# Performance work log

Hardware: AMD Instinct MI355X
Metric: run time of the kernel (lower is better)

Reference implementation:

```python
import jax, jax.numpy as jnp
import numpy as np

N_SEQ = 250000
L = 40
C_IN = 20
K = 4
D = 32
N_BAGS = 100
SEQ_PER_BAG = N_SEQ // N_BAGS


def _param(key, shape):
    # matches torch init: normal(0, sqrt(1/prod(shape)))
    return jax.random.normal(key, shape, dtype=jnp.float32) * np.sqrt(1.0 / np.prod(shape))


def setup_inputs() -> dict:
    key = jax.random.key(0)
    ks = jax.random.split(key, 16)
    inp = {
        "x": jax.random.normal(ks[0], (N_SEQ, L, C_IN), dtype=jnp.float32),
        # equal-size bags: 100 bags of 2500 sequences (sum == N_SEQ)
        "n_per_bag": jnp.full((N_BAGS,), SEQ_PER_BAG, dtype=jnp.int32),
        # CNN: two conv1d layers, kernel shape (K, in, out) for 'NWC'/'WIO'
        "conv1_w": _param(ks[1], (K, C_IN, D)), "conv1_b": jnp.zeros((D,), jnp.float32),
        "conv2_w": _param(ks[2], (K, D, D)),    "conv2_b": jnp.zeros((D,), jnp.float32),
        # attention MLP: 32->32->32->1
        "att_w1": _param(ks[3], (D, D)), "att_b1": jnp.zeros((D,), jnp.float32),
        "att_w2": _param(ks[4], (D, D)), "att_b2": jnp.zeros((D,), jnp.float32),
        "att_w3": _param(ks[5], (D, 1)), "att_b3": jnp.zeros((1,), jnp.float32),
        # output net A: 32->32->21, output net B: 32->32->40
        "outA_w1": _param(ks[6], (D, D)),  "outA_b1": jnp.zeros((D,), jnp.float32),
        "outA_w2": _param(ks[7], (D, 21)), "outA_b2": jnp.zeros((21,), jnp.float32),
        "outB_w1": _param(ks[8], (D, D)),  "outB_b1": jnp.zeros((D,), jnp.float32),
        "outB_w2": _param(ks[9], (D, 40)), "outB_b2": jnp.zeros((40,), jnp.float32),
    }
    return inp


def _conv1d_nwc(x, w, b):
    # x: (N, L, Cin), w: (K, Cin, Cout) -> (N, L-K+1, Cout), VALID padding
    return jax.lax.conv_general_dilated(
        x, w, window_strides=(1,), padding="VALID",
        dimension_numbers=("NWC", "WIO", "NWC")) + b


def _forward(x, n_per_bag, conv1_w, conv1_b, conv2_w, conv2_b,
             att_w1, att_b1, att_w2, att_b2, att_w3, att_b3,
             outA_w1, outA_b1, outA_w2, outA_b2,
             outB_w1, outB_b1, outB_w2, outB_b2):
    selu = jax.nn.selu
    # --- sequence embedding CNN (dropout = identity in eval) ---
    h = selu(_conv1d_nwc(x, conv1_w, conv1_b))          # (N, L-3, D)
    h = selu(_conv1d_nwc(h, conv2_w, conv2_b))          # (N, L-6, D)
    seq_embed = h.max(axis=1)                           # (N, D)
    # --- attention scores ---
    a = selu(seq_embed @ att_w1 + att_b1)
    a = selu(a @ att_w2 + att_b2)
    scores = (a @ att_w3 + att_b3)[:, 0]                # (N,)
    # --- per-bag segment softmax + weighted-sum pooling ---
    seg = jnp.repeat(jnp.arange(N_BAGS, dtype=jnp.int32), np.asarray(n_per_bag),
                     total_repeat_length=seq_embed.shape[0])
    seg_max = jax.ops.segment_max(scores, seg, num_segments=N_BAGS)
    e = jnp.exp(scores - seg_max[seg])
    denom = jax.ops.segment_sum(e, seg, num_segments=N_BAGS)
    w = e / denom[seg]                                  # (N,)
    pooled = jax.ops.segment_sum(seq_embed * w[:, None], seg,
                                 num_segments=N_BAGS)   # (N_BAGS, D)
    # --- output networks (n_layers=2: one hidden SELU layer + final, then sigmoid) ---
    pa = jax.nn.sigmoid(selu(pooled @ outA_w1 + outA_b1) @ outA_w2 + outA_b2)
    pb = jax.nn.sigmoid(selu(pooled @ outB_w1 + outB_b1) @ outB_w2 + outB_b2)
    return pa, pb


def reference(x, n_per_bag, conv1_w, conv1_b, conv2_w, conv2_b,
              att_w1, att_b1, att_w2, att_b2, att_w3, att_b3,
              outA_w1, outA_b1, outA_w2, outA_b2,
              outB_w1, outB_b1, outB_w2, outB_b2):
    return _forward(x, n_per_bag, conv1_w, conv1_b, conv2_w, conv2_b,
                    att_w1, att_b1, att_w2, att_b2, att_w3, att_b3,
                    outA_w1, outA_b1, outA_w2, outA_b2,
                    outB_w1, outB_b1, outB_w2, outB_b2)
```

## Files before the change

### kernel.cpp

```cpp
#include <hip/hip_runtime.h>

#define N_SEQ 250000
#define LSEQ  40
#define CIN   20
#define KW    4
#define DCH   32
#define L1    37
#define L2    34
#define N_BAGS 100
#define SPB   2500
#define NTHR  256
#define WPB   4
#define H1S   40

typedef _Float16 f16;
typedef _Float16 f16x8 __attribute__((ext_vector_type(8)));
typedef _Float16 f16x4 __attribute__((ext_vector_type(4)));
typedef float    f32x16 __attribute__((ext_vector_type(16)));

__device__ __forceinline__ float selu_f(float x) {
  float e = 1.6732632423543772f * (__expf(x) - 1.0f);
  return 1.0507009873554805f * ((x > 0.0f) ? x : e);
}

__device__ __forceinline__ float lane_bcast(float v, int srclane) {
  return __int_as_float(__builtin_amdgcn_readlane(__float_as_int(v), srclane));
}

__global__ __launch_bounds__(256) void prep_kernel(
    const float* __restrict__ w1, const float* __restrict__ w2,
    const float* __restrict__ aw1, const float* __restrict__ aw2,
    f16* __restrict__ w1T, f16* __restrict__ w2T,
    float* __restrict__ aw1T, float* __restrict__ aw2T)
{
  const int tid = threadIdx.x;
  for (int i = tid; i < 32 * 80; i += 256) {
    const int n = i / 80, k = i - n * 80;
    w1T[i] = (f16)w1[k * 32 + n];
  }
  for (int i = tid; i < 32 * 128; i += 256) {
    const int n = i >> 7, k = i & 127;
    w2T[i] = (f16)w2[k * 32 + n];
  }
  for (int i = tid; i < 1024; i += 256) {
    const int d = i >> 5, c = i & 31;
    aw1T[i] = aw1[c * 32 + d];
    aw2T[i] = aw2[c * 32 + d];
  }
}

__global__ __launch_bounds__(NTHR, 4) void seq_kernel(
    const float* __restrict__ x,
    const f16*  __restrict__ w1T, const float* __restrict__ b1,
    const f16*  __restrict__ w2T, const float* __restrict__ b2,
    const float* __restrict__ aw1T, const float* __restrict__ ab1,
    const float* __restrict__ aw2T, const float* __restrict__ ab2,
    const float* __restrict__ aw3, const float* __restrict__ ab3,
    f16* __restrict__ se_out, float* __restrict__ sc_out)
{
  __shared__ __align__(16) f16 xs[WPB][LSEQ * CIN];
  __shared__ __align__(16) f16 h1[WPB][L1 * H1S];

  const int tid  = threadIdx.x;
  const int lane = tid & 63;
  const int wave = tid >> 6;
  const int m    = lane & 31;
  const int half = lane >> 5;
  const int seq  = blockIdx.x * WPB + wave;

  f16* xw  = xs[wave];
  f16* h1w = h1[wave];

  {
    const float4* xg = (const float4*)(x + (size_t)seq * (LSEQ * CIN));
    for (int i = lane; i < 100; i += 64) {
      const float4 v0 = xg[2 * i];
      const float4 v1 = xg[2 * i + 1];
      f16x8 h;
      h[0] = (f16)v0.x; h[1] = (f16)v0.y; h[2] = (f16)v0.z; h[3] = (f16)v0.w;
      h[4] = (f16)v1.x; h[5] = (f16)v1.y; h[6] = (f16)v1.z; h[7] = (f16)v1.w;
      *(f16x8*)&xw[i * 8] = h;
    }
  }

  f16x8 bf1[5];
  {
    const f16x8* w1t8 = (const f16x8*)w1T;
    #pragma unroll
    for (int kc = 0; kc < 5; kc++) bf1[kc] = w1t8[m * 10 + kc * 2 + half];
  }
  const float b1v = b1[m];

  #pragma unroll
  for (int tile = 0; tile < 2; tile++) {
    const int l = tile ? min(32 + m, L1 - 1) : m;
    const f16* arow = &xw[l * CIN];
    f32x16 acc;
    #pragma unroll
    for (int i = 0; i < 16; i++) acc[i] = b1v;
    #pragma unroll
    for (int kc = 0; kc < 5; kc++) {
      const int e = kc * 16 + half * 8;
      const f16x4 p0 = *(const f16x4*)(arow + e);
      const f16x4 p1 = *(const f16x4*)(arow + e + 4);
      const f16x8 a = __builtin_shufflevector(p0, p1, 0, 1, 2, 3, 4, 5, 6, 7);
      acc = __builtin_amdgcn_mfma_f32_32x32x16_f16(a, bf1[kc], acc, 0, 0, 0);
    }
    if (tile == 0) {
      #pragma unroll
      for (int reg = 0; reg < 16; reg++) {
        const int rr = (reg & 3) + 8 * (reg >> 2) + 4 * half;
        h1w[rr * H1S + m] = (f16)selu_f(acc[reg]);
      }
    } else {
      if (half == 0) {
        #pragma unroll
        for (int reg = 0; reg < 4; reg++)
          h1w[(32 + reg) * H1S + m] = (f16)selu_f(acc[reg]);
      } else {
        h1w[36 * H1S + m] = (f16)selu_f(acc[0]);
      }
    }
  }

  f16x8 bf2[8];
  {
    const f16x8* w2t8 = (const f16x8*)w2T;
    #pragma unroll
    for (int kc = 0; kc < 8; kc++) bf2[kc] = w2t8[m * 16 + kc * 2 + half];
  }
  const float b2v = b2[m];

  float mx = -3.4e38f;
  #pragma unroll
  for (int tile = 0; tile < 2; tile++) {
    const int l = tile ? min(32 + m, L2 - 1) : m;
    const f16* abase = &h1w[l * H1S];
    f32x16 acc;
    #pragma unroll
    for (int i = 0; i < 16; i++) acc[i] = 0.0f;
    #pragma unroll
    for (int kc = 0; kc < 8; kc++) {
      const int e = (kc >> 1) * H1S + (kc & 1) * 16 + half * 8;
      const f16x8 a = *(const f16x8*)(abase + e);
      acc = __builtin_amdgcn_mfma_f32_32x32x16_f16(a, bf2[kc], acc, 0, 0, 0);
    }
    if (tile == 0) {
      #pragma unroll
      for (int reg = 0; reg < 16; reg++) mx = fmaxf(mx, acc[reg]);
    } else if (half == 0) {
      mx = fmaxf(mx, fmaxf(acc[0], acc[1]));
    }
  }
  mx = fmaxf(mx, __shfl_xor(mx, 32, 64));
  const float sv = selu_f(mx + b2v);
  if (half == 0) se_out[(size_t)seq * DCH + m] = (f16)sv;

  {
    const float4* wt1 = (const float4*)aw1T;
    float a = ab1[m];
    #pragma unroll
    for (int c4 = 0; c4 < 8; c4++) {
      const float4 w = wt1[m * 8 + c4];
      a = fmaf(lane_bcast(sv, c4 * 4 + 0), w.x, a);
      a = fmaf(lane_bcast(sv, c4 * 4 + 1), w.y, a);
      a = fmaf(lane_bcast(sv, c4 * 4 + 2), w.z, a);
      a = fmaf(lane_bcast(sv, c4 * 4 + 3), w.w, a);
    }
    const float av = selu_f(a);

    const float4* wt2 = (const float4*)aw2T;
    float a2 = ab2[m];
    #pragma unroll
    for (int c4 = 0; c4 < 8; c4++) {
      const float4 w = wt2[m * 8 + c4];
      a2 = fmaf(lane_bcast(av, c4 * 4 + 0), w.x, a2);
      a2 = fmaf(lane_bcast(av, c4 * 4 + 1), w.y, a2);
      a2 = fmaf(lane_bcast(av, c4 * 4 + 2), w.z, a2);
      a2 = fmaf(lane_bcast(av, c4 * 4 + 3), w.w, a2);
    }
    float p = selu_f(a2) * aw3[m];
    #pragma unroll
    for (int off = 16; off > 0; off >>= 1) p += __shfl_xor(p, off, 32);
    if (lane == 0) sc_out[seq] = p + ab3[0];
  }
}

__global__ __launch_bounds__(256) void bag_kernel(
    const f16* __restrict__ se, const float* __restrict__ sc,
    const float* __restrict__ aw1, const float* __restrict__ ab1,
    const float* __restrict__ aw2, const float* __restrict__ ab2,
    const float* __restrict__ bw1, const float* __restrict__ bb1,
    const float* __restrict__ bw2, const float* __restrict__ bb2,
    float* __restrict__ out)
{
  const int bag = blockIdx.x, tid = threadIdx.x;
  const size_t base = (size_t)bag * SPB;

  __shared__ float pr[4][33];
  __shared__ float red[33];
  __shared__ float pool[DCH], hA[DCH], hB[DCH];

  float m = -3.4e38f;
  for (int i = tid; i < SPB; i += 256) m = fmaxf(m, sc[base + i]);
  #pragma unroll
  for (int off = 32; off > 0; off >>= 1) m = fmaxf(m, __shfl_xor(m, off, 64));
  if ((tid & 63) == 0) pr[tid >> 6][0] = m;
  __syncthreads();
  const float bagmax = fmaxf(fmaxf(pr[0][0], pr[1][0]), fmaxf(pr[2][0], pr[3][0]));
  __syncthreads();

  float acc[33];
  #pragma unroll
  for (int d = 0; d < 33; d++) acc[d] = 0.0f;
  for (int i = tid; i < SPB; i += 256) {
    const float e = __expf(sc[base + i] - bagmax);
    acc[32] += e;
    const f16* sr = &se[(base + i) * DCH];
    #pragma unroll
    for (int q = 0; q < 8; q++) {
      const f16x4 v = *(const f16x4*)(sr + q * 4);
      #pragma unroll
      for (int j = 0; j < 4; j++) acc[q * 4 + j] = fmaf(e, (float)v[j], acc[q * 4 + j]);
    }
  }
  #pragma unroll
  for (int d = 0; d < 33; d++) {
    float v = acc[d];
    #pragma unroll
    for (int off = 32; off > 0; off >>= 1) v += __shfl_xor(v, off, 64);
    if ((tid & 63) == 0) pr[tid >> 6][d] = v;
  }
  __syncthreads();
  if (tid < 33) red[tid] = pr[0][tid] + pr[1][tid] + pr[2][tid] + pr[3][tid];
  __syncthreads();
  if (tid < DCH) pool[tid] = red[tid] / red[32];
  __syncthreads();

  if (tid < DCH) {
    float a = ab1[tid], b = bb1[tid];
    #pragma unroll
    for (int c = 0; c < DCH; c++) {
      a = fmaf(pool[c], aw1[c * DCH + tid], a);
      b = fmaf(pool[c], bw1[c * DCH + tid], b);
    }
    hA[tid] = selu_f(a);
    hB[tid] = selu_f(b);
  }
  __syncthreads();

  if (tid < 21) {
    float v = ab2[tid];
    #pragma unroll
    for (int d = 0; d < DCH; d++) v = fmaf(hA[d], aw2[d * 21 + tid], v);
    out[bag * 21 + tid] = 1.0f / (1.0f + __expf(-v));
  } else if (tid >= 32 && tid < 72) {
    const int j = tid - 32;
    float v = bb2[j];
    #pragma unroll
    for (int d = 0; d < DCH; d++) v = fmaf(hB[d], bw2[d * 40 + j], v);
    out[N_BAGS * 21 + bag * 40 + j] = 1.0f / (1.0f + __expf(-v));
  }
}

extern "C" void kernel_launch(void* const* d_in, const int* in_sizes, int n_in,
                              void* d_out, int out_size, void* d_ws, size_t ws_size,
                              hipStream_t stream)
{
  const float* x    = (const float*)d_in[0];
  const float* c1w  = (const float*)d_in[2];
  const float* c1b  = (const float*)d_in[3];
  const float* c2w  = (const float*)d_in[4];
  const float* c2b  = (const float*)d_in[5];
  const float* aw1  = (const float*)d_in[6];
  const float* ab1  = (const float*)d_in[7];
  const float* aw2  = (const float*)d_in[8];
  const float* ab2  = (const float*)d_in[9];
  const float* aw3  = (const float*)d_in[10];
  const float* ab3  = (const float*)d_in[11];
  const float* oaw1 = (const float*)d_in[12];
  const float* oab1 = (const float*)d_in[13];
  const float* oaw2 = (const float*)d_in[14];
  const float* oab2 = (const float*)d_in[15];
  const float* obw1 = (const float*)d_in[16];
  const float* obb1 = (const float*)d_in[17];
  const float* obw2 = (const float*)d_in[18];
  const float* obb2 = (const float*)d_in[19];
  float* out = (float*)d_out;

  char* ws = (char*)d_ws;
  f16*   seh  = (f16*)ws;
  float* sc   = (float*)(ws + (size_t)16000000);
  f16*   w1T  = (f16*)(ws + (size_t)17000000);
  f16*   w2T  = w1T + 2560 + 2560;
  float* aw1T = (float*)(ws + (size_t)17000000 + 32768);
  float* aw2T = aw1T + 1024;

  prep_kernel<<<1, 256, 0, stream>>>(c1w, c2w, aw1, aw2, w1T, w2T, aw1T, aw2T);
  seq_kernel<<<N_SEQ / WPB, NTHR, 0, stream>>>(x, w1T, c1b, w2T, c2b,
                                               aw1T, ab1, aw2T, ab2, aw3, ab3,
                                               seh, sc);
  bag_kernel<<<N_BAGS, 256, 0, stream>>>(seh, sc, oaw1, oab1, oaw2, oab2,
                                         obw1, obb1, obw2, obb2, out);
}
```

Baseline: 1.602 ms.

## Make seq kernel persistent with register prefetch of next sequence

The sequence kernel changes from one block per four sequences (62500 blocks) to a persistent grid of 1024 blocks. Each wave loops over sequences and loads the next sequence's input into registers while it computes the current one. Conv weight fragments and attention weights are loaded once per block, with the attention MLP weights staged in LDS. This removes per-block launch and weight-reload overhead and hides global-load latency, at the cost of more registers and fewer total waves to hide latency.

```diff
diff --git a/kernel.cpp b/kernel.cpp
--- a/kernel.cpp
+++ b/kernel.cpp
@@ -11,6 +11,8 @@
 #define SPB   2500
 #define NTHR  256
 #define WPB   4
+#define NBLK  1024
+#define NWAVES (NBLK * WPB)
 #define H1S   40
 
 typedef _Float16 f16;
@@ -60,129 +62,155 @@
 {
   __shared__ __align__(16) f16 xs[WPB][LSEQ * CIN];
   __shared__ __align__(16) f16 h1[WPB][L1 * H1S];
+  __shared__ float4 awl1[256];
+  __shared__ float4 awl2[256];
 
   const int tid  = threadIdx.x;
   const int lane = tid & 63;
   const int wave = tid >> 6;
   const int m    = lane & 31;
   const int half = lane >> 5;
-  const int seq  = blockIdx.x * WPB + wave;
+
+  {
+    const int c4 = tid >> 5, d = tid & 31;
+    awl1[tid] = ((const float4*)aw1T)[d * 8 + c4];
+    awl2[tid] = ((const float4*)aw2T)[d * 8 + c4];
+  }
+  __syncthreads();
+
+  f16x8 bf1[5], bf2[8];
+  {
+    const f16x8* w1t8 = (const f16x8*)w1T;
+    #pragma unroll
+    for (int kc = 0; kc < 5; kc++) bf1[kc] = w1t8[m * 10 + kc * 2 + half];
+    const f16x8* w2t8 = (const f16x8*)w2T;
+    #pragma unroll
+    for (int kc = 0; kc < 8; kc++) bf2[kc] = w2t8[m * 16 + kc * 2 + half];
+  }
+  const float b1v  = b1[m],  b2v  = b2[m];
+  const float ab1v = ab1[m], ab2v = ab2[m];
+  const float aw3v = aw3[m], ab3v = ab3[0];
 
   f16* xw  = xs[wave];
   f16* h1w = h1[wave];
 
+  const int gwid = blockIdx.x * WPB + wave;
+
+  float4 c0, c1, c2, c3;
   {
-    const float4* xg = (const float4*)(x + (size_t)seq * (LSEQ * CIN));
-    for (int i = lane; i < 100; i += 64) {
-      const float4 v0 = xg[2 * i];
-      const float4 v1 = xg[2 * i + 1];
+    const float4* xg = (const float4*)(x + (size_t)gwid * (LSEQ * CIN));
+    c0 = xg[2 * lane]; c1 = xg[2 * lane + 1];
+    if (lane < 36) { c2 = xg[2 * (lane + 64)]; c3 = xg[2 * (lane + 64) + 1]; }
+  }
+
+  #pragma unroll 1
+  for (int s = gwid; s < N_SEQ; s += NWAVES) {
+    const int sn = s + NWAVES;
+    float4 n0, n1, n2, n3;
+    if (sn < N_SEQ) {
+      const float4* xg = (const float4*)(x + (size_t)sn * (LSEQ * CIN));
+      n0 = xg[2 * lane]; n1 = xg[2 * lane + 1];
+      if (lane < 36) { n2 = xg[2 * (lane + 64)]; n3 = xg[2 * (lane + 64) + 1]; }
+    }
+
+    {
       f16x8 h;
-      h[0] = (f16)v0.x; h[1] = (f16)v0.y; h[2] = (f16)v0.z; h[3] = (f16)v0.w;
-      h[4] = (f16)v1.x; h[5] = (f16)v1.y; h[6] = (f16)v1.z; h[7] = (f16)v1.w;
-      *(f16x8*)&xw[i * 8] = h;
-    }
-  }
-
-  f16x8 bf1[5];
-  {
-    const f16x8* w1t8 = (const f16x8*)w1T;
-    #pragma unroll
-    for (int kc = 0; kc < 5; kc++) bf1[kc] = w1t8[m * 10 + kc * 2 + half];
-  }
-  const float b1v = b1[m];
-
-  #pragma unroll
-  for (int tile = 0; tile < 2; tile++) {
-    const int l = tile ? min(32 + m, L1 - 1) : m;
-    const f16* arow = &xw[l * CIN];
-    f32x16 acc;
-    #pragma unroll
-    for (int i = 0; i < 16; i++) acc[i] = b1v;
-    #pragma unroll
-    for (int kc = 0; kc < 5; kc++) {
-      const int e = kc * 16 + half * 8;
-      const f16x4 p0 = *(const f16x4*)(arow + e);
-      const f16x4 p1 = *(const f16x4*)(arow + e + 4);
-      const f16x8 a = __builtin_shufflevector(p0, p1, 0, 1, 2, 3, 4, 5, 6, 7);
-      acc = __builtin_amdgcn_mfma_f32_32x32x16_f16(a, bf1[kc], acc, 0, 0, 0);
-    }
-    if (tile == 0) {
-      #pragma unroll
-      for (int reg = 0; reg < 16; reg++) {
-        const int rr = (reg & 3) + 8 * (reg >> 2) + 4 * half;
-        h1w[rr * H1S + m] = (f16)selu_f(acc[reg]);
-      }
-    } else {
-      if (half == 0) {
+      h[0] = (f16)c0.x; h[1] = (f16)c0.y; h[2] = (f16)c0.z; h[3] = (f16)c0.w;
+      h[4] = (f16)c1.x; h[5] = (f16)c1.y; h[6] = (f16)c1.z; h[7] = (f16)c1.w;
+      *(f16x8*)&xw[lane * 8] = h;
+      if (lane < 36) {
+        f16x8 g;
+        g[0] = (f16)c2.x; g[1] = (f16)c2.y; g[2] = (f16)c2.z; g[3] = (f16)c2.w;
+        g[4] = (f16)c3.x; g[5] = (f16)c3.y; g[6] = (f16)c3.z; g[7] = (f16)c3.w;
+        *(f16x8*)&xw[(lane + 64) * 8] = g;
+      }
+    }
+
+    #pragma unroll
+    for (int tile = 0; tile < 2; tile++) {
+      const int l = tile ? min(32 + m, L1 - 1) : m;
+      const f16* arow = &xw[l * CIN];
+      f32x16 acc;
+      #pragma unroll
+      for (int i = 0; i < 16; i++) acc[i] = b1v;
+      #pragma unroll
+      for (int kc = 0; kc < 5; kc++) {
+        const int e = kc * 16 + half * 8;
+        const f16x4 p0 = *(const f16x4*)(arow + e);
+        const f16x4 p1 = *(const f16x4*)(arow + e + 4);
+        const f16x8 a = __builtin_shufflevector(p0, p1, 0, 1, 2, 3, 4, 5, 6, 7);
+        acc = __builtin_amdgcn_mfma_f32_32x32x16_f16(a, bf1[kc], acc, 0, 0, 0);
+      }
+      if (tile == 0) {
         #pragma unroll
-        for (int reg = 0; reg < 4; reg++)
-          h1w[(32 + reg) * H1S + m] = (f16)selu_f(acc[reg]);
+        for (int reg = 0; reg < 16; reg++) {
+          const int rr = (reg & 3) + 8 * (reg >> 2) + 4 * half;
+          h1w[rr * H1S + m] = (f16)selu_f(acc[reg]);
+        }
       } else {
-        h1w[36 * H1S + m] = (f16)selu_f(acc[0]);
-      }
-    }
-  }
-
-  f16x8 bf2[8];
-  {
-    const f16x8* w2t8 = (const f16x8*)w2T;
-    #pragma unroll
-    for (int kc = 0; kc < 8; kc++) bf2[kc] = w2t8[m * 16 + kc * 2 + half];
-  }
-  const float b2v = b2[m];
-
-  float mx = -3.4e38f;
-  #pragma unroll
-  for (int tile = 0; tile < 2; tile++) {
-    const int l = tile ? min(32 + m, L2 - 1) : m;
-    const f16* abase = &h1w[l * H1S];
-    f32x16 acc;
-    #pragma unroll
-    for (int i = 0; i < 16; i++) acc[i] = 0.0f;
-    #pragma unroll
-    for (int kc = 0; kc < 8; kc++) {
-      const int e = (kc >> 1) * H1S + (kc & 1) * 16 + half * 8;
-      const f16x8 a = *(const f16x8*)(abase + e);
-      acc = __builtin_amdgcn_mfma_f32_32x32x16_f16(a, bf2[kc], acc, 0, 0, 0);
-    }
-    if (tile == 0) {
-      #pragma unroll
-      for (int reg = 0; reg < 16; reg++) mx = fmaxf(mx, acc[reg]);
-    } else if (half == 0) {
-      mx = fmaxf(mx, fmaxf(acc[0], acc[1]));
-    }
-  }
-  mx = fmaxf(mx, __shfl_xor(mx, 32, 64));
-  const float sv = selu_f(mx + b2v);
-  if (half == 0) se_out[(size_t)seq * DCH + m] = (f16)sv;
-
-  {
-    const float4* wt1 = (const float4*)aw1T;
-    float a = ab1[m];
-    #pragma unroll
-    for (int c4 = 0; c4 < 8; c4++) {
-      const float4 w = wt1[m * 8 + c4];
-      a = fmaf(lane_bcast(sv, c4 * 4 + 0), w.x, a);
-      a = fmaf(lane_bcast(sv, c4 * 4 + 1), w.y, a);
-      a = fmaf(lane_bcast(sv, c4 * 4 + 2), w.z, a);
-      a = fmaf(lane_bcast(sv, c4 * 4 + 3), w.w, a);
-    }
-    const float av = selu_f(a);
-
-    const float4* wt2 = (const float4*)aw2T;
-    float a2 = ab2[m];
-    #pragma unroll
-    for (int c4 = 0; c4 < 8; c4++) {
-      const float4 w = wt2[m * 8 + c4];
-      a2 = fmaf(lane_bcast(av, c4 * 4 + 0), w.x, a2);
-      a2 = fmaf(lane_bcast(av, c4 * 4 + 1), w.y, a2);
-      a2 = fmaf(lane_bcast(av, c4 * 4 + 2), w.z, a2);
-      a2 = fmaf(lane_bcast(av, c4 * 4 + 3), w.w, a2);
-    }
-    float p = selu_f(a2) * aw3[m];
-    #pragma unroll
-    for (int off = 16; off > 0; off >>= 1) p += __shfl_xor(p, off, 32);
-    if (lane == 0) sc_out[seq] = p + ab3[0];
+        if (half == 0) {
+          #pragma unroll
+          for (int reg = 0; reg < 4; reg++)
+            h1w[(32 + reg) * H1S + m] = (f16)selu_f(acc[reg]);
+        } else {
+          h1w[36 * H1S + m] = (f16)selu_f(acc[0]);
+        }
+      }
+    }
+
+    float mx = -3.4e38f;
+    #pragma unroll
+    for (int tile = 0; tile < 2; tile++) {
+      const int l = tile ? min(32 + m, L2 - 1) : m;
+      const f16* abase = &h1w[l * H1S];
+      f32x16 acc;
+      #pragma unroll
+      for (int i = 0; i < 16; i++) acc[i] = 0.0f;
+      #pragma unroll
+      for (int kc = 0; kc < 8; kc++) {
+        const int e = (kc >> 1) * H1S + (kc & 1) * 16 + half * 8;
+        const f16x8 a = *(const f16x8*)(abase + e);
+        acc = __builtin_amdgcn_mfma_f32_32x32x16_f16(a, bf2[kc], acc, 0, 0, 0);
+      }
+      if (tile == 0) {
+        #pragma unroll
+        for (int reg = 0; reg < 16; reg++) mx = fmaxf(mx, acc[reg]);
+      } else if (half == 0) {
+        mx = fmaxf(mx, fmaxf(acc[0], acc[1]));
+      }
+    }
+    mx = fmaxf(mx, __shfl_xor(mx, 32, 64));
+    const float sv = selu_f(mx + b2v);
+    if (half == 0) se_out[(size_t)s * DCH + m] = (f16)sv;
+
+    {
+      float a = ab1v;
+      #pragma unroll
+      for (int c4 = 0; c4 < 8; c4++) {
+        const float4 w = awl1[c4 * 32 + m];
+        a = fmaf(lane_bcast(sv, c4 * 4 + 0), w.x, a);
+        a = fmaf(lane_bcast(sv, c4 * 4 + 1), w.y, a);
+        a = fmaf(lane_bcast(sv, c4 * 4 + 2), w.z, a);
+        a = fmaf(lane_bcast(sv, c4 * 4 + 3), w.w, a);
+      }
+      const float av = selu_f(a);
+
+      float a2 = ab2v;
+      #pragma unroll
+      for (int c4 = 0; c4 < 8; c4++) {
+        const float4 w = awl2[c4 * 32 + m];
+        a2 = fmaf(lane_bcast(av, c4 * 4 + 0), w.x, a2);
+        a2 = fmaf(lane_bcast(av, c4 * 4 + 1), w.y, a2);
+        a2 = fmaf(lane_bcast(av, c4 * 4 + 2), w.z, a2);
+        a2 = fmaf(lane_bcast(av, c4 * 4 + 3), w.w, a2);
+      }
+      float p = selu_f(a2) * aw3v;
+      #pragma unroll
+      for (int off = 16; off > 0; off >>= 1) p += __shfl_xor(p, off, 32);
+      if (lane == 0) sc_out[s] = p + ab3v;
+    }
+
+    c0 = n0; c1 = n1; c2 = n2; c3 = n3;
   }
 }
 
@@ -297,9 +325,9 @@
   float* aw2T = aw1T + 1024;
 
   prep_kernel<<<1, 256, 0, stream>>>(c1w, c2w, aw1, aw2, w1T, w2T, aw1T, aw2T);
-  seq_kernel<<<N_SEQ / WPB, NTHR, 0, stream>>>(x, w1T, c1b, w2T, c2b,
-                                               aw1T, ab1, aw2T, ab2, aw3, ab3,
-                                               seh, sc);
+  seq_kernel<<<NBLK, NTHR, 0, stream>>>(x, w1T, c1b, w2T, c2b,
+                                        aw1T, ab1, aw2T, ab2, aw3, ab3,
+                                        seh, sc);
   bag_kernel<<<N_BAGS, 256, 0, stream>>>(seh, sc, oaw1, oab1, oaw2, oab2,
                                          obw1, obb1, obw2, obb2, out);
 }
```

Result: slower. 2.072 ms (+29.4%).
